# Kernel tuning notes

Measured on AMD Instinct MI355X. Metric: run time of the kernel, lower is better.

The kernel has to match this reference:

```python
import jax, jax.numpy as jnp
import numpy as np

BOHR_RADIUS = 0.529177  # Angstrom
KE_KCAL = 332.0636      # Coulomb constant, kcal/mol * Angstrom / e^2
EPS = 1e-15
R_CUT = 5.0

ZBL = {'d': [0.8854 * BOHR_RADIUS], 'z_exp': [0.23],
       'c': [0.1818, 0.5099, 0.2802, 0.02817],
       'exponents': [3.2, 0.9423, 0.4028, 0.2016]}

def _inv_softplus(v):
    v = np.asarray(v, dtype=np.float32)
    return jnp.asarray(np.log(np.exp(v) - 1.0).reshape(-1, 1))

def setup_inputs() -> dict:
    key = jax.random.key(0)
    k1, k2, k3, k4 = jax.random.split(key, 4)
    N, E, M = 200000, 8000000, 1000
    xyz = jax.random.normal(k1, (N, 3), dtype=jnp.float32) * 3.0
    z = jax.random.randint(k2, (N,), 1, 94, dtype=jnp.int32)
    nbrs = jax.random.randint(k3, (E, 2), 0, N, dtype=jnp.int32)
    offsets = jax.random.normal(k4, (E, 3), dtype=jnp.float32) * 2.0
    num_atoms = jnp.full((M,), N // M, dtype=jnp.int32)
    return {
        'xyz': xyz, 'z': z, 'nbrs': nbrs, 'num_atoms': num_atoms, 'offsets': offsets,
        'd_inv': _inv_softplus(ZBL['d']),
        'z_exp_inv': _inv_softplus(ZBL['z_exp']),
        'c_inv': _inv_softplus(ZBL['c']),
        'exponents_inv': _inv_softplus(ZBL['exponents']),
    }

def reference(xyz, z, nbrs, num_atoms, offsets, d_inv, z_exp_inv, c_inv, exponents_inv):
    sp = jax.nn.softplus
    d, z_exp, c, exponents = sp(d_inv), sp(z_exp_inv), sp(c_inv), sp(exponents_inv)

    i, j = nbrs[:, 0], nbrs[:, 1]
    mask = j > i  # undirected-edge filter (masked instead of gathered: same math)

    z_i = z[i].astype(jnp.float32)  # [E]
    z_j = z[j].astype(jnp.float32)
    diff = xyz[i] - xyz[j] - offsets                  # [E,3]
    r_ij = jnp.sqrt((diff ** 2 + EPS).sum(-1))        # stable norm, [E]

    # ZBL phi: d,z_exp are [1,1]; broadcast over edges
    a = (d / (z_i ** z_exp + z_j ** z_exp)).reshape(-1)           # [E]
    phi = (c * jnp.exp(-exponents * r_ij / a)).sum(0) / c.sum()   # [4,E] -> [E]

    # SpookyNet cutoff, NaN-safe outside r_cut
    den = (R_CUT - r_ij) * (R_CUT + r_ij)
    safe_den = jnp.where(r_ij < R_CUT, den, 1.0)
    f_cut = jnp.where(r_ij < R_CUT, jnp.exp(-r_ij ** 2 / safe_den), 0.0)

    pairwise = KE_KCAL * z_i * z_j / r_ij * phi * f_cut
    pairwise = jnp.where(mask, pairwise, 0.0)

    N = xyz.shape[0]
    M = num_atoms.shape[0]
    mol_idx = jnp.repeat(jnp.arange(M), num_atoms, total_repeat_length=N)  # [N]
    seg = mol_idx[i]                                                       # [E]
    energy = jax.ops.segment_sum(pairwise, seg, num_segments=M).reshape(-1, 1)
    return energy
```

## Files before the change

### kernel.cpp

```cpp
#include <hip/hip_runtime.h>
#include <hip/hip_bf16.h>

#define KE_F  332.0636f
#define MAX_M 1024
#define BLK   256
#define NBLK  2048

typedef int   ivec4 __attribute__((ext_vector_type(4)));
typedef float fvec4 __attribute__((ext_vector_type(4)));

__device__ __forceinline__ float softplusf(float x) {
    return logf(1.0f + expf(x));
}

__global__ void scan_params_kernel(const int* __restrict__ num_atoms, int M,
                                   const float* __restrict__ d_inv,
                                   const float* __restrict__ z_exp_inv,
                                   const float* __restrict__ c_inv,
                                   const float* __restrict__ exp_inv,
                                   int* __restrict__ mol_starts,
                                   float* __restrict__ params,
                                   float* __restrict__ out) {
    __shared__ int buf[MAX_M];
    int t = threadIdx.x;
    buf[t] = (t < M) ? num_atoms[t] : 0;
    __syncthreads();
    for (int off = 1; off < MAX_M; off <<= 1) {
        int x = (t >= off) ? buf[t - off] : 0;
        __syncthreads();
        buf[t] += x;
        __syncthreads();
    }
    if (t == 0) mol_starts[0] = 0;
    if (t < M) mol_starts[t + 1] = buf[t];
    if (t == 0) {
        float dd = softplusf(d_inv[0]);
        float c0 = softplusf(c_inv[0]), c1 = softplusf(c_inv[1]);
        float c2 = softplusf(c_inv[2]), c3 = softplusf(c_inv[3]);
        float e0 = softplusf(exp_inv[0]), e1 = softplusf(exp_inv[1]);
        float e2 = softplusf(exp_inv[2]), e3 = softplusf(exp_inv[3]);
        float ic = 1.0f / (c0 + c1 + c2 + c3);
        float id = 1.0f / dd;
        params[0] = c0 * ic; params[1] = c1 * ic; params[2] = c2 * ic; params[3] = c3 * ic;
        params[4] = e0 * id; params[5] = e1 * id; params[6] = e2 * id; params[7] = e3 * id;
    }
    if (t < 96) {
        float zexp = softplusf(z_exp_inv[0]);
        params[16 + t] = __powf((float)t, zexp);
    }
    for (int k = t; k < M; k += MAX_M) out[k] = 0.0f;
}

__global__ void pack_kernel(const float* __restrict__ xyz,
                            const int* __restrict__ z,
                            const int* __restrict__ mol_starts, int M, int N,
                            float4* __restrict__ pack) {
    int a = blockIdx.x * blockDim.x + threadIdx.x;
    if (a >= N) return;
    int lo = 0, hi = M;
    while (hi - lo > 1) {
        int mid = (lo + hi) >> 1;
        if (mol_starts[mid] <= a) lo = mid; else hi = mid;
    }
    pack[a] = make_float4(xyz[3 * a + 0], xyz[3 * a + 1], xyz[3 * a + 2],
                          (float)((lo << 7) | z[a]));
}

__global__ __launch_bounds__(BLK) void nr_main_kernel(
    const int* __restrict__ nbrs, const float* __restrict__ offsets,
    const float4* __restrict__ pack,
    const float* __restrict__ params, float* __restrict__ out, int E, int M) {
    __shared__ float sm[MAX_M];
    __shared__ float zp[96];
    for (int t = threadIdx.x; t < MAX_M; t += BLK) sm[t] = 0.0f;
    if (threadIdx.x < 96) zp[threadIdx.x] = params[16 + threadIdx.x];
    __syncthreads();

    const float4 kk = *(const float4*)(params + 0);
    const float4 gg = *(const float4*)(params + 4);

    const int ngroups = E >> 2;
    const int stride = gridDim.x * BLK;
    const ivec4* nb4 = (const ivec4*)nbrs;
    const fvec4* of4 = (const fvec4*)offsets;

    for (int g = blockIdx.x * BLK + threadIdx.x; g < ngroups; g += stride) {
        const ivec4 n01 = __builtin_nontemporal_load(nb4 + 2 * (size_t)g);
        const ivec4 n23 = __builtin_nontemporal_load(nb4 + 2 * (size_t)g + 1);
        const fvec4 oA  = __builtin_nontemporal_load(of4 + 3 * (size_t)g);
        const fvec4 oB  = __builtin_nontemporal_load(of4 + 3 * (size_t)g + 1);
        const fvec4 oC  = __builtin_nontemporal_load(of4 + 3 * (size_t)g + 2);

        const int   iv[4] = {n01.x, n01.z, n23.x, n23.z};
        const int   jv[4] = {n01.y, n01.w, n23.y, n23.w};
        const float ox[4] = {oA.x, oA.w, oB.z, oC.y};
        const float oy[4] = {oA.y, oB.x, oB.w, oC.z};
        const float oz[4] = {oA.z, oB.y, oC.x, oC.w};

        bool   m[4];
        float4 pi[4], pj[4];
#pragma unroll
        for (int k = 0; k < 4; ++k) {
            m[k] = jv[k] > iv[k];
            const int ii = m[k] ? iv[k] : 0;
            const int jj = m[k] ? jv[k] : 0;
            pi[k] = pack[ii];
            pj[k] = pack[jj];
        }
#pragma unroll
        for (int k = 0; k < 4; ++k) {
            const float dx = pi[k].x - pj[k].x - ox[k];
            const float dy = pi[k].y - pj[k].y - oy[k];
            const float dz = pi[k].z - pj[k].z - oz[k];
            const float r2 = fmaf(dx, dx, fmaf(dy, dy, dz * dz)) + 3e-15f;
            const bool ok = m[k] && (r2 < 25.0f);
            const int  wi = (int)pi[k].w;
            const int  wj = (int)pj[k].w;
            const float zi = (float)(wi & 127);
            const float zj = (float)(wj & 127);
            const float inv_r = rsqrtf(r2);
            const float r = r2 * inv_r;
            const float S = zp[wi & 127] + zp[wj & 127];
            const float rs = r * S;
            const float phi = kk.x * __expf(-gg.x * rs) + kk.y * __expf(-gg.y * rs) +
                              kk.z * __expf(-gg.z * rs) + kk.w * __expf(-gg.w * rs);
            const float fc = __expf(-__fdividef(r2, 25.0f - r2));
            const float val = KE_F * zi * zj * inv_r * phi * fc;
            if (ok) atomicAdd(&sm[wi >> 7], val);
        }
    }

    for (int e = (ngroups << 2) + blockIdx.x * BLK + threadIdx.x; e < E; e += stride) {
        const int i = nbrs[2 * e], j = nbrs[2 * e + 1];
        if (j <= i) continue;
        const float oxs = offsets[3 * e], oys = offsets[3 * e + 1], ozs = offsets[3 * e + 2];
        const float4 pis = pack[i], pjs = pack[j];
        const float dx = pis.x - pjs.x - oxs;
        const float dy = pis.y - pjs.y - oys;
        const float dz = pis.z - pjs.z - ozs;
        const float r2 = fmaf(dx, dx, fmaf(dy, dy, dz * dz)) + 3e-15f;
        if (r2 >= 25.0f) continue;
        const int  wi = (int)pis.w;
        const int  wj = (int)pjs.w;
        const float inv_r = rsqrtf(r2);
        const float r = r2 * inv_r;
        const float S = zp[wi & 127] + zp[wj & 127];
        const float rs = r * S;
        const float phi = kk.x * __expf(-gg.x * rs) + kk.y * __expf(-gg.y * rs) +
                          kk.z * __expf(-gg.z * rs) + kk.w * __expf(-gg.w * rs);
        const float fc = __expf(-__fdividef(r2, 25.0f - r2));
        atomicAdd(&sm[wi >> 7],
                  KE_F * (float)(wi & 127) * (float)(wj & 127) * inv_r * phi * fc);
    }

    __syncthreads();
    for (int t = threadIdx.x; t < M; t += BLK) {
        const float v = sm[t];
        if (v != 0.0f) atomicAdd(&out[t], v);
    }
}

extern "C" void kernel_launch(void* const* d_in, const int* in_sizes, int n_in,
                              void* d_out, int out_size, void* d_ws, size_t ws_size,
                              hipStream_t stream) {
    const float* xyz       = (const float*)d_in[0];
    const int*   z         = (const int*)d_in[1];
    const int*   nbrs      = (const int*)d_in[2];
    const int*   num_atoms = (const int*)d_in[3];
    const float* offsets   = (const float*)d_in[4];
    const float* d_inv     = (const float*)d_in[5];
    const float* z_exp_inv = (const float*)d_in[6];
    const float* c_inv     = (const float*)d_in[7];
    const float* exp_inv   = (const float*)d_in[8];
    float* out = (float*)d_out;

    const int N = in_sizes[0] / 3;
    const int E = in_sizes[2] / 2;
    const int M = in_sizes[3];

    char* w = (char*)d_ws;
    int*    mol_starts = (int*)w;
    float*  params     = (float*)(w + 4096);
    float4* pack       = (float4*)(w + 8192);

    scan_params_kernel<<<1, MAX_M, 0, stream>>>(num_atoms, M, d_inv, z_exp_inv,
                                                c_inv, exp_inv, mol_starts,
                                                params, out);
    pack_kernel<<<(N + BLK - 1) / BLK, BLK, 0, stream>>>(xyz, z, mol_starts, M, N,
                                                         pack);
    nr_main_kernel<<<NBLK, BLK, 0, stream>>>(nbrs, offsets, pack,
                                             params, out, E, M);
}
```

Measured before the change: 249.2 us.

## Software-pipeline edge loop with double-buffered streaming and gather loads

Restructures the main edge loop into a two-stage software pipeline. The streaming loads for the next groups and the pack gathers for the following group are issued before the math for the current group runs, so gather latency overlaps with compute. Grid size is halved and launch bounds are set for 4 waves per SIMD to pay for the extra live registers. The risks are higher register pressure, lower occupancy, and less parallelism from the smaller grid.

Result: slower. 254.2 us (+2.0%).

```diff
diff --git a/kernel.cpp b/kernel.cpp
--- a/kernel.cpp
+++ b/kernel.cpp
@@ -4,7 +4,7 @@
 #define KE_F  332.0636f
 #define MAX_M 1024
 #define BLK   256
-#define NBLK  2048
+#define NBLK  1024
 
 typedef int   ivec4 __attribute__((ext_vector_type(4)));
 typedef float fvec4 __attribute__((ext_vector_type(4)));
@@ -66,7 +66,7 @@
                           (float)((lo << 7) | z[a]));
 }
 
-__global__ __launch_bounds__(BLK) void nr_main_kernel(
+__global__ __launch_bounds__(BLK, 4) void nr_main_kernel(
     const int* __restrict__ nbrs, const float* __restrict__ offsets,
     const float4* __restrict__ pack,
     const float* __restrict__ params, float* __restrict__ out, int E, int M) {
@@ -80,55 +80,93 @@
     const float4 gg = *(const float4*)(params + 4);
 
     const int ngroups = E >> 2;
-    const int stride = gridDim.x * BLK;
+    const int stride  = gridDim.x * BLK;
     const ivec4* nb4 = (const ivec4*)nbrs;
     const fvec4* of4 = (const fvec4*)offsets;
 
-    for (int g = blockIdx.x * BLK + threadIdx.x; g < ngroups; g += stride) {
-        const ivec4 n01 = __builtin_nontemporal_load(nb4 + 2 * (size_t)g);
-        const ivec4 n23 = __builtin_nontemporal_load(nb4 + 2 * (size_t)g + 1);
-        const fvec4 oA  = __builtin_nontemporal_load(of4 + 3 * (size_t)g);
-        const fvec4 oB  = __builtin_nontemporal_load(of4 + 3 * (size_t)g + 1);
-        const fvec4 oC  = __builtin_nontemporal_load(of4 + 3 * (size_t)g + 2);
-
-        const int   iv[4] = {n01.x, n01.z, n23.x, n23.z};
-        const int   jv[4] = {n01.y, n01.w, n23.y, n23.w};
-        const float ox[4] = {oA.x, oA.w, oB.z, oC.y};
-        const float oy[4] = {oA.y, oB.x, oB.w, oC.z};
-        const float oz[4] = {oA.z, oB.y, oC.x, oC.w};
-
-        bool   m[4];
-        float4 pi[4], pj[4];
-#pragma unroll
-        for (int k = 0; k < 4; ++k) {
-            m[k] = jv[k] > iv[k];
-            const int ii = m[k] ? iv[k] : 0;
-            const int jj = m[k] ? jv[k] : 0;
-            pi[k] = pack[ii];
-            pj[k] = pack[jj];
+#define LOAD_S(g, N01, N23, O0, O1, O2) do {                                  \
+        const size_t _c = (size_t)((g) < ngroups ? (g) : ngroups - 1);        \
+        N01 = __builtin_nontemporal_load(nb4 + 2 * _c);                       \
+        N23 = __builtin_nontemporal_load(nb4 + 2 * _c + 1);                   \
+        O0  = __builtin_nontemporal_load(of4 + 3 * _c);                       \
+        O1  = __builtin_nontemporal_load(of4 + 3 * _c + 1);                   \
+        O2  = __builtin_nontemporal_load(of4 + 3 * _c + 2);                   \
+    } while (0)
+
+#define ISSUE_G(g, N01, N23, O0, O1, O2, MB, PI, PJ, OX, OY, OZ) do {         \
+        const bool _v = (g) < ngroups;                                        \
+        const int _i0 = N01.x, _i1 = N01.z, _i2 = N23.x, _i3 = N23.z;         \
+        const int _j0 = N01.y, _j1 = N01.w, _j2 = N23.y, _j3 = N23.w;         \
+        const bool _m0 = _v && (_j0 > _i0), _m1 = _v && (_j1 > _i1);          \
+        const bool _m2 = _v && (_j2 > _i2), _m3 = _v && (_j3 > _i3);          \
+        MB = (int)_m0 | ((int)_m1 << 1) | ((int)_m2 << 2) | ((int)_m3 << 3);  \
+        PI[0] = pack[_m0 ? _i0 : 0]; PJ[0] = pack[_m0 ? _j0 : 0];             \
+        PI[1] = pack[_m1 ? _i1 : 0]; PJ[1] = pack[_m1 ? _j1 : 0];             \
+        PI[2] = pack[_m2 ? _i2 : 0]; PJ[2] = pack[_m2 ? _j2 : 0];             \
+        PI[3] = pack[_m3 ? _i3 : 0]; PJ[3] = pack[_m3 ? _j3 : 0];             \
+        OX[0] = O0.x; OX[1] = O0.w; OX[2] = O1.z; OX[3] = O2.y;               \
+        OY[0] = O0.y; OY[1] = O1.x; OY[2] = O1.w; OY[3] = O2.z;               \
+        OZ[0] = O0.z; OZ[1] = O1.y; OZ[2] = O2.x; OZ[3] = O2.w;               \
+    } while (0)
+
+#define MATH_G(MB, PI, PJ, OX, OY, OZ) do {                                   \
+        _Pragma("unroll")                                                     \
+        for (int k = 0; k < 4; ++k) {                                         \
+            const float dx = PI[k].x - PJ[k].x - OX[k];                       \
+            const float dy = PI[k].y - PJ[k].y - OY[k];                       \
+            const float dz = PI[k].z - PJ[k].z - OZ[k];                       \
+            const float r2 = fmaf(dx, dx, fmaf(dy, dy, dz * dz)) + 3e-15f;    \
+            const bool ok = (((MB) >> k) & 1) && (r2 < 25.0f);                \
+            const int  wi = (int)PI[k].w;                                     \
+            const int  wj = (int)PJ[k].w;                                     \
+            const float zi = (float)(wi & 127);                               \
+            const float zj = (float)(wj & 127);                               \
+            const float inv_r = rsqrtf(r2);                                   \
+            const float r = r2 * inv_r;                                       \
+            const float S = zp[wi & 127] + zp[wj & 127];                      \
+            const float rs = r * S;                                           \
+            const float phi = kk.x * __expf(-gg.x * rs) + kk.y * __expf(-gg.y * rs) + \
+                              kk.z * __expf(-gg.z * rs) + kk.w * __expf(-gg.w * rs);  \
+            const float fc = __expf(-__fdividef(r2, 25.0f - r2));             \
+            const float val = KE_F * zi * zj * inv_r * phi * fc;              \
+            if (ok) atomicAdd(&sm[wi >> 7], val);                             \
+        }                                                                     \
+    } while (0)
+
+    if (ngroups > 0) {
+        const int ITER = (ngroups + stride - 1) / stride;
+        int gA = blockIdx.x * BLK + threadIdx.x;
+        int gB = gA + stride;
+
+        ivec4 aN01, aN23; fvec4 aO0, aO1, aO2;
+        ivec4 bN01, bN23; fvec4 bO0, bO1, bO2;
+        float4 api[4], apj[4], bpi[4], bpj[4];
+        float  aox[4], aoy[4], aoz[4], box[4], boy[4], boz[4];
+        int    amb, bmb;
+
+        LOAD_S(gA, aN01, aN23, aO0, aO1, aO2);
+        LOAD_S(gB, bN01, bN23, bO0, bO1, bO2);
+        ISSUE_G(gA, aN01, aN23, aO0, aO1, aO2, amb, api, apj, aox, aoy, aoz);
+
+        for (int it = 0; ; it += 2) {
+            const int gC = gA + 2 * stride;
+            const int gD = gB + 2 * stride;
+            const bool more = (it + 2 < ITER);
+            ISSUE_G(gB, bN01, bN23, bO0, bO1, bO2, bmb, bpi, bpj, box, boy, boz);
+            if (more) LOAD_S(gC, aN01, aN23, aO0, aO1, aO2);
+            MATH_G(amb, api, apj, aox, aoy, aoz);
+            if (more) {
+                ISSUE_G(gC, aN01, aN23, aO0, aO1, aO2, amb, api, apj, aox, aoy, aoz);
+                LOAD_S(gD, bN01, bN23, bO0, bO1, bO2);
+            }
+            MATH_G(bmb, bpi, bpj, box, boy, boz);
+            if (!more) break;
+            gA = gC; gB = gD;
         }
-#pragma unroll
-        for (int k = 0; k < 4; ++k) {
-            const float dx = pi[k].x - pj[k].x - ox[k];
-            const float dy = pi[k].y - pj[k].y - oy[k];
-            const float dz = pi[k].z - pj[k].z - oz[k];
-            const float r2 = fmaf(dx, dx, fmaf(dy, dy, dz * dz)) + 3e-15f;
-            const bool ok = m[k] && (r2 < 25.0f);
-            const int  wi = (int)pi[k].w;
-            const int  wj = (int)pj[k].w;
-            const float zi = (float)(wi & 127);
-            const float zj = (float)(wj & 127);
-            const float inv_r = rsqrtf(r2);
-            const float r = r2 * inv_r;
-            const float S = zp[wi & 127] + zp[wj & 127];
-            const float rs = r * S;
-            const float phi = kk.x * __expf(-gg.x * rs) + kk.y * __expf(-gg.y * rs) +
-                              kk.z * __expf(-gg.z * rs) + kk.w * __expf(-gg.w * rs);
-            const float fc = __expf(-__fdividef(r2, 25.0f - r2));
-            const float val = KE_F * zi * zj * inv_r * phi * fc;
-            if (ok) atomicAdd(&sm[wi >> 7], val);
-        }
-    }
+    }
+#undef LOAD_S
+#undef ISSUE_G
+#undef MATH_G
 
     for (int e = (ngroups << 2) + blockIdx.x * BLK + threadIdx.x; e < E; e += stride) {
         const int i = nbrs[2 * e], j = nbrs[2 * e + 1];
```

## Coalesce edge loads per wavefront and transpose offsets through LDS

Applied to the files above, without the earlier changes.

Each wavefront now takes a 256-edge chunk. It loads the neighbor pairs as contiguous 8-byte words per lane and the offsets as contiguous 16-byte vectors, then transposes the offsets through a per-wave shared-memory buffer so each lane gets its own edge's xyz offset. This replaces the earlier per-thread strided 16-byte loads of four consecutive edges, aiming for fully coalesced global access. The cost is LDS stores, reads with a stride of 3 (possible bank conflicts), wave barriers, and extra shared memory per block.

Measured after the change: 240.9 us, median of 2. -3.3%, faster.

```diff
diff --git a/kernel.cpp b/kernel.cpp
--- a/kernel.cpp
+++ b/kernel.cpp
@@ -1,16 +1,23 @@
 #include <hip/hip_runtime.h>
 #include <hip/hip_bf16.h>
 
-#define KE_F  332.0636f
-#define MAX_M 1024
-#define BLK   256
-#define NBLK  2048
-
+#define KE_F   332.0636f
+#define MAX_M  1024
+#define BLK    256
+#define NBLK   2048
+#define WCHUNK 256
+
+typedef int   ivec2 __attribute__((ext_vector_type(2)));
 typedef int   ivec4 __attribute__((ext_vector_type(4)));
 typedef float fvec4 __attribute__((ext_vector_type(4)));
 
 __device__ __forceinline__ float softplusf(float x) {
     return logf(1.0f + expf(x));
+}
+
+__device__ __forceinline__ void wave_fence() {
+    __builtin_amdgcn_wave_barrier();
+    asm volatile("" ::: "memory");
 }
 
 __global__ void scan_params_kernel(const int* __restrict__ num_atoms, int M,
@@ -72,6 +79,7 @@
     const float* __restrict__ params, float* __restrict__ out, int E, int M) {
     __shared__ float sm[MAX_M];
     __shared__ float zp[96];
+    __shared__ float sof[4][WCHUNK * 3];
     for (int t = threadIdx.x; t < MAX_M; t += BLK) sm[t] = 0.0f;
     if (threadIdx.x < 96) zp[threadIdx.x] = params[16 + threadIdx.x];
     __syncthreads();
@@ -79,43 +87,55 @@
     const float4 kk = *(const float4*)(params + 0);
     const float4 gg = *(const float4*)(params + 4);
 
-    const int ngroups = E >> 2;
-    const int stride = gridDim.x * BLK;
-    const ivec4* nb4 = (const ivec4*)nbrs;
+    const int lane = threadIdx.x & 63;
+    float* myof = sof[threadIdx.x >> 6];
+
+    const int nchunks = E / WCHUNK;
+    const int gw = (blockIdx.x * BLK + threadIdx.x) >> 6;
+    const int nw = (gridDim.x * BLK) >> 6;
+
+    const ivec2* nbp = (const ivec2*)nbrs;
     const fvec4* of4 = (const fvec4*)offsets;
 
-    for (int g = blockIdx.x * BLK + threadIdx.x; g < ngroups; g += stride) {
-        const ivec4 n01 = __builtin_nontemporal_load(nb4 + 2 * (size_t)g);
-        const ivec4 n23 = __builtin_nontemporal_load(nb4 + 2 * (size_t)g + 1);
-        const fvec4 oA  = __builtin_nontemporal_load(of4 + 3 * (size_t)g);
-        const fvec4 oB  = __builtin_nontemporal_load(of4 + 3 * (size_t)g + 1);
-        const fvec4 oC  = __builtin_nontemporal_load(of4 + 3 * (size_t)g + 2);
-
-        const int   iv[4] = {n01.x, n01.z, n23.x, n23.z};
-        const int   jv[4] = {n01.y, n01.w, n23.y, n23.w};
-        const float ox[4] = {oA.x, oA.w, oB.z, oC.y};
-        const float oy[4] = {oA.y, oB.x, oB.w, oC.z};
-        const float oz[4] = {oA.z, oB.y, oC.x, oC.w};
+    for (int c = gw; c < nchunks; c += nw) {
+        const size_t eb = (size_t)c * WCHUNK;
+        ivec2 nb[4];
+#pragma unroll
+        for (int h = 0; h < 4; ++h)
+            nb[h] = __builtin_nontemporal_load(nbp + eb + 64 * h + lane);
+        const fvec4* ofb = of4 + (size_t)c * ((WCHUNK * 3) / 4);
+        const fvec4 F0 = __builtin_nontemporal_load(ofb + lane);
+        const fvec4 F1 = __builtin_nontemporal_load(ofb + 64 + lane);
+        const fvec4 F2 = __builtin_nontemporal_load(ofb + 128 + lane);
 
         bool   m[4];
         float4 pi[4], pj[4];
 #pragma unroll
-        for (int k = 0; k < 4; ++k) {
-            m[k] = jv[k] > iv[k];
-            const int ii = m[k] ? iv[k] : 0;
-            const int jj = m[k] ? jv[k] : 0;
-            pi[k] = pack[ii];
-            pj[k] = pack[jj];
+        for (int h = 0; h < 4; ++h) {
+            const int iv = nb[h].x, jv = nb[h].y;
+            m[h] = jv > iv;
+            pi[h] = pack[m[h] ? iv : 0];
+            pj[h] = pack[m[h] ? jv : 0];
         }
+
+        wave_fence();
+        *(fvec4*)&myof[4 * lane]       = F0;
+        *(fvec4*)&myof[4 * lane + 256] = F1;
+        *(fvec4*)&myof[4 * lane + 512] = F2;
+        wave_fence();
+
 #pragma unroll
-        for (int k = 0; k < 4; ++k) {
-            const float dx = pi[k].x - pj[k].x - ox[k];
-            const float dy = pi[k].y - pj[k].y - oy[k];
-            const float dz = pi[k].z - pj[k].z - oz[k];
+        for (int h = 0; h < 4; ++h) {
+            const float oxv = myof[192 * h + 3 * lane + 0];
+            const float oyv = myof[192 * h + 3 * lane + 1];
+            const float ozv = myof[192 * h + 3 * lane + 2];
+            const float dx = pi[h].x - pj[h].x - oxv;
+            const float dy = pi[h].y - pj[h].y - oyv;
+            const float dz = pi[h].z - pj[h].z - ozv;
             const float r2 = fmaf(dx, dx, fmaf(dy, dy, dz * dz)) + 3e-15f;
-            const bool ok = m[k] && (r2 < 25.0f);
-            const int  wi = (int)pi[k].w;
-            const int  wj = (int)pj[k].w;
+            const bool ok = m[h] && (r2 < 25.0f);
+            const int  wi = (int)pi[h].w;
+            const int  wj = (int)pj[h].w;
             const float zi = (float)(wi & 127);
             const float zj = (float)(wj & 127);
             const float inv_r = rsqrtf(r2);
@@ -130,7 +150,8 @@
         }
     }
 
-    for (int e = (ngroups << 2) + blockIdx.x * BLK + threadIdx.x; e < E; e += stride) {
+    const int stride = gridDim.x * BLK;
+    for (int e = nchunks * WCHUNK + blockIdx.x * BLK + threadIdx.x; e < E; e += stride) {
         const int i = nbrs[2 * e], j = nbrs[2 * e + 1];
         if (j <= i) continue;
         const float oxs = offsets[3 * e], oys = offsets[3 * e + 1], ozs = offsets[3 * e + 2];
```
